# Kernel tuning notes

Hardware: AMD Instinct MI355X
Metric: run time of the kernel (lower is better)

Reference implementation:

```python
import jax, jax.numpy as jnp
import numpy as np

N_NODES = 50000


def gcn_conv_max(x, edge_index, edge_weight, W, b):
    """PyG GCNConv with aggr='max': gcn_norm (add self-loops, symmetric
    degree normalization), linear transform, gather-scale-scatter_max, bias."""
    n = x.shape[0]
    row, col = edge_index[0], edge_index[1]
    loop = jnp.arange(n)
    row = jnp.concatenate([row, loop])  # sources (incl. self-loops)
    col = jnp.concatenate([col, loop])  # targets
    ew = jnp.concatenate([edge_weight, jnp.ones((n,), x.dtype)])
    deg = jax.ops.segment_sum(ew, col, num_segments=n)
    dis = jnp.where(deg > 0, jax.lax.rsqrt(deg), jnp.zeros_like(deg))
    norm = dis[row] * ew * dis[col]  # [E+N]
    h = x @ W                         # [N, out]
    msg = norm[:, None] * h[row]      # gather + scale, [E+N, out]
    agg = jax.ops.segment_max(msg, col, num_segments=n)  # scatter-max
    return agg + b


def setup_inputs() -> dict:
    key = jax.random.key(0)
    ks = jax.random.split(key, 9)
    N, E = N_NODES, 1_600_000
    x = jax.random.normal(ks[0], (N, 5), dtype=jnp.float32)
    edge_index = jax.random.randint(ks[1], (2, E), 0, N, dtype=jnp.int64)
    edge_weight = jax.random.uniform(ks[2], (E,), dtype=jnp.float32)
    s1 = 1.0 / np.sqrt(5.0)
    s2 = 1.0 / np.sqrt(240.0)
    W1 = jax.random.uniform(ks[3], (5, 240), jnp.float32, -s1, s1)
    b1 = jnp.zeros((240,), jnp.float32)
    W2 = jax.random.uniform(ks[4], (240, 240), jnp.float32, -s2, s2)
    b2 = jnp.zeros((240,), jnp.float32)
    We = jax.random.uniform(ks[5], (240, 80), jnp.float32, -s2, s2)
    be = jnp.zeros((80,), jnp.float32)
    return {"x": x, "edge_index": edge_index, "edge_weight": edge_weight,
            "W1": W1, "b1": b1, "W2": W2, "b2": b2, "We": We, "be": be}


def reference(x, edge_index, edge_weight, W1, b1, W2, b2, We, be):
    h = gcn_conv_max(x, edge_index, edge_weight, W1, b1)
    h = jax.nn.relu(h)
    h = gcn_conv_max(h, edge_index, edge_weight, W2, b2)
    h = jax.nn.relu(h)
    return h @ We + be  # [N, 80]
```

## Files before the change

### kernel.cpp

```cpp
#include <hip/hip_runtime.h>
#include <cfloat>

#define HID 240

static inline size_t alignUp(size_t x, size_t a){ return (x + a - 1) / a * a; }

typedef __bf16 bf16x8 __attribute__((ext_vector_type(8)));
typedef unsigned short u16x8 __attribute__((ext_vector_type(8)));
typedef float  f32x16 __attribute__((ext_vector_type(16)));
typedef float  f32x4  __attribute__((ext_vector_type(4)));

__device__ __forceinline__ float b2f(unsigned short u){
    return __uint_as_float(((unsigned)u) << 16);
}
__device__ __forceinline__ unsigned short f2b_rne(float f){
    unsigned r = __float_as_uint(f);
    r += 0x7FFFu + ((r >> 16) & 1u);
    return (unsigned short)(r >> 16);
}
__device__ __forceinline__ float max3f(float a, float b, float c){
    return fmaxf(fmaxf(a, b), c);
}

__device__ __forceinline__ float vmax16(f32x16 a){
    float x0 = fmaxf(fmaxf(a[0],  a[1]),  a[2]);
    float x1 = fmaxf(fmaxf(a[3],  a[4]),  a[5]);
    float x2 = fmaxf(fmaxf(a[6],  a[7]),  a[8]);
    float x3 = fmaxf(fmaxf(a[9],  a[10]), a[11]);
    float x4 = fmaxf(fmaxf(a[12], a[13]), a[14]);
    float y0 = fmaxf(fmaxf(x0, x1), x2);
    float y1 = fmaxf(fmaxf(x3, x4), a[15]);
    return fmaxf(y0, y1);
}

__global__ void k_deg_prep(const int* __restrict__ col, const float* __restrict__ ew,
                           unsigned long long* __restrict__ pk, unsigned* __restrict__ rank,
                           int E, int ne, int N, int nb,
                           const float* __restrict__ x, float* __restrict__ xp,
                           const float* __restrict__ W1, unsigned short* __restrict__ W1f,
                           const float* __restrict__ W2, unsigned short* __restrict__ Bt2h,
                           unsigned short* __restrict__ Bt2l,
                           const float* __restrict__ We, unsigned short* __restrict__ Bt3h,
                           unsigned short* __restrict__ Bt3l){
    int b = blockIdx.x;
    int t = threadIdx.x;
    if (b < ne){
        int e = b * 256 + t;
        if (e < E){
            int c = col[e];
            unsigned q = __float2uint_rn(ew[e] * 1048576.0f);
            unsigned long long old = atomicAdd(&pk[c], (1ull << 40) | (unsigned long long)q);
            rank[e] = (unsigned)(old >> 40);
        }
        return;
    }
    int bb = b - ne;
    if (bb < nb){
        __shared__ float s[1280];
        int rbase = bb * 256;
        #pragma unroll
        for (int c = 0; c < 5; c++){
            int idx = rbase * 5 + t + 256 * c;
            s[t + 256 * c] = (idx < N * 5) ? x[idx] : 0.0f;
        }
        __syncthreads();
        #pragma unroll
        for (int c = 0; c < 8; c++){
            int pos = t + 256 * c;
            int r = pos >> 3, j = pos & 7;
            int grow = rbase + r;
            if (grow < N)
                xp[(size_t)grow * 8 + j] = (j < 5) ? s[r * 5 + j] : 0.0f;
        }
        return;
    }
    bb -= nb;
    if (bb < 32){
        int i = bb * 256 + t;
        if (i < 2 * 8 * 64 * 8){
            int k    = i & 7;
            int lane = (i >> 3) & 63;
            int j    = (i >> 9) & 7;
            int s2   = i >> 12;
            int lm = lane & 31, quad = lane >> 5;
            int kg = quad * 8 + k;
            int colm = 32 * j + lm;
            float v = (kg < 5 && colm < HID) ? W1[kg * HID + colm] : 0.0f;
            unsigned short hi = f2b_rne(v);
            W1f[i] = (s2 == 0) ? hi : f2b_rne(v - b2f(hi));
        }
        return;
    }
    bb -= 32;
    if (bb < 240){
        int i = bb * 256 + t;
        int n = i / HID, k = i - n * HID;
        float v = (n < HID) ? W2[(size_t)k * HID + n] : 0.0f;
        unsigned short hi = f2b_rne(v);
        Bt2h[i] = hi;
        Bt2l[i] = f2b_rne(v - b2f(hi));
        return;
    }
    bb -= 240;
    {
        int i = bb * 256 + t;
        if (i < 128 * HID){
            int n = i / HID, k = i - n * HID;
            float v = (n < 80) ? We[(size_t)k * 80 + n] : 0.0f;
            unsigned short hi = f2b_rne(v);
            Bt3h[i] = hi;
            Bt3l[i] = f2b_rne(v - b2f(hi));
        }
    }
}

__global__ void k_dis_bsum(const unsigned long long* __restrict__ pk,
                           float* __restrict__ dis, unsigned* __restrict__ cnt,
                           unsigned* __restrict__ bsum, int N){
    int b = blockIdx.x;
    int i = b * 256 + threadIdx.x;
    unsigned v = 0u;
    if (i < N){
        unsigned long long p = pk[i];
        unsigned c = (unsigned)(p >> 40);
        cnt[i] = c;
        float deg = 1.0f + (float)(p & 0xFFFFFFFFFFull) * (1.0f / 1048576.0f);
        dis[i] = rsqrtf(deg);
        v = (c + 32u) >> 5;
    }
    #pragma unroll
    for (int o = 32; o > 0; o >>= 1) v += __shfl_down(v, (unsigned)o, 64);
    __shared__ unsigned ws[4];
    int lane = threadIdx.x & 63, w = threadIdx.x >> 6;
    if (lane == 0) ws[w] = v;
    __syncthreads();
    if (threadIdx.x == 0) bsum[b] = ws[0] + ws[1] + ws[2] + ws[3];
}

__global__ void k_bscan(const unsigned* __restrict__ bsum, unsigned* __restrict__ boff,
                        unsigned* __restrict__ poff, int nb, int N){
    __shared__ unsigned s[256];
    int t = threadIdx.x;
    unsigned v = (t < nb) ? bsum[t] : 0u;
    s[t] = v;
    __syncthreads();
    for (int o = 1; o < 256; o <<= 1){
        unsigned u = (t >= o) ? s[t - o] : 0u;
        __syncthreads();
        s[t] += u;
        __syncthreads();
    }
    if (t < nb) boff[t] = s[t] - v;
    if (t == 0) poff[N] = 32u * s[nb - 1];
}

__global__ void k_offs_fill(const unsigned* __restrict__ cnt, const unsigned* __restrict__ boff,
                            const float* __restrict__ dis,
                            unsigned* __restrict__ poff, int2* __restrict__ sedge, int N){
    int b = blockIdx.x, t = threadIdx.x;
    int i = b * 256 + t;
    unsigned c = (i < N) ? cnt[i] : 0u;
    unsigned v = (i < N) ? ((c + 32u) >> 5) : 0u;
    int lane = t & 63, w = t >> 6;
    unsigned x = v;
    #pragma unroll
    for (int o = 1; o < 64; o <<= 1){
        unsigned u = __shfl_up(x, (unsigned)o, 64);
        if (lane >= o) x += u;
    }
    __shared__ unsigned ws[4];
    if (lane == 63) ws[w] = x;
    __syncthreads();
    unsigned wb = 0;
    if (w > 0) wb += ws[0];
    if (w > 1) wb += ws[1];
    if (w > 2) wb += ws[2];
    if (i < N){
        unsigned p = 32u * (boff[b] + wb + x - v);
        poff[i] = p;
        float dd = dis[i];
        int2 sv = make_int2(i, __float_as_int(dd * dd));
        sedge[p] = sv;
        unsigned s1 = p + 32u * v;
        for (unsigned s = p + 1u + c; s < s1; s++) sedge[s] = sv;
    }
}

__global__ void k_scatter(const int* __restrict__ row, const int* __restrict__ col,
                          const float* __restrict__ ew, const float* __restrict__ dis,
                          const unsigned* __restrict__ poff, const unsigned* __restrict__ rank,
                          int2* __restrict__ sedge, int E){
    int e = blockIdx.x * blockDim.x + threadIdx.x;
    if (e < E){
        int r = row[e], c = col[e];
        float nw = dis[r] * ew[e] * dis[c];
        unsigned p = poff[c] + 1u + rank[e];
        sedge[p] = make_int2(r, __float_as_int(nw));
    }
}

__global__ __launch_bounds__(256) void k_agg1m(const float* __restrict__ xp,
                                               const unsigned short* __restrict__ W1f,
                                               const unsigned* __restrict__ cnt,
                                               const unsigned* __restrict__ poff,
                                               const int2* __restrict__ sedge,
                                               const float* __restrict__ bias,
                                               float* __restrict__ out, int N, int nwaves){
    int wid  = blockIdx.x * 4 + (threadIdx.x >> 6);
    int lane = threadIdx.x & 63;
    int lm   = lane & 31;

    bf16x8 bh[8], bl[8];
    #pragma unroll
    for (int j = 0; j < 8; j++){
        bh[j] = *(const bf16x8*)(W1f + ((size_t)(0 * 8 + j) * 64 + lane) * 8);
        bl[j] = *(const bf16x8*)(W1f + ((size_t)(1 * 8 + j) * 64 + lane) * 8);
    }
    float bv[8];
    #pragma unroll
    for (int j = 0; j < 8; j++){
        int c = 32 * j + lm;
        bv[j] = (c < HID) ? bias[c] : 0.0f;
    }
    const f32x16 zv = {};

    for (int d = wid; d < N; d += nwaves){
        unsigned base = poff[d];
        unsigned nch  = (cnt[d] + 32u) >> 5;
        float m[8];
        #pragma unroll
        for (int j = 0; j < 8; j++) m[j] = -FLT_MAX;

        for (unsigned c = 0; c < nch; c++){
            u16x8 ahu = (u16x8)0, alu = (u16x8)0;
            if (lane < 32){
                int2 e = sedge[base + 32u * c + (unsigned)lm];
                float w = __int_as_float(e.y);
                const float4* xr = (const float4*)(xp + (size_t)e.x * 8);
                float4 x0 = xr[0], x1 = xr[1];
                float p[5] = {w * x0.x, w * x0.y, w * x0.z, w * x0.w, w * x1.x};
                #pragma unroll
                for (int k = 0; k < 5; k++){
                    unsigned short h = f2b_rne(p[k]);
                    ahu[k] = h;
                    alu[k] = f2b_rne(p[k] - b2f(h));
                }
            }
            bf16x8 ah = __builtin_bit_cast(bf16x8, ahu);
            bf16x8 al = __builtin_bit_cast(bf16x8, alu);
            #pragma unroll
            for (int j = 0; j < 8; j += 2){
                f32x16 a0 = __builtin_amdgcn_mfma_f32_32x32x16_bf16(ah, bh[j],     zv, 0, 0, 0);
                f32x16 a1 = __builtin_amdgcn_mfma_f32_32x32x16_bf16(ah, bh[j + 1], zv, 0, 0, 0);
                a0 = __builtin_amdgcn_mfma_f32_32x32x16_bf16(ah, bl[j],     a0, 0, 0, 0);
                a1 = __builtin_amdgcn_mfma_f32_32x32x16_bf16(ah, bl[j + 1], a1, 0, 0, 0);
                a0 = __builtin_amdgcn_mfma_f32_32x32x16_bf16(al, bh[j],     a0, 0, 0, 0);
                a1 = __builtin_amdgcn_mfma_f32_32x32x16_bf16(al, bh[j + 1], a1, 0, 0, 0);
                m[j]     = fmaxf(m[j],     vmax16(a0));
                m[j + 1] = fmaxf(m[j + 1], vmax16(a1));
            }
        }
        float o[8];
        #pragma unroll
        for (int j = 0; j < 8; j++){
            float other = __shfl_xor(m[j], 32, 64);
            o[j] = fmaxf(fmaxf(m[j], other) + bv[j], 0.0f);
        }
        if (lane < 32){
            float* orow = out + (size_t)d * HID;
            #pragma unroll
            for (int j = 0; j < 8; j++){
                int c = 32 * j + lm;
                if (c < HID) orow[c] = o[j];
            }
        }
    }
}

template <bool OB16>
__global__ __launch_bounds__(256) void k_gemm_mfma(const float* __restrict__ A,
                                                   const unsigned short* __restrict__ Bth,
                                                   const unsigned short* __restrict__ Btl,
                                                   const float* __restrict__ bias,
                                                   void* __restrict__ Cv,
                                                   int M, int Ncol, int Npad, int Cld){
    __shared__ unsigned short As_hi[64][24];
    __shared__ unsigned short As_lo[64][24];
    const int K = 240;
    int t = threadIdx.x;
    int wave = t >> 6, lane = t & 63;
    int m0 = blockIdx.x * 64;
    int n0 = wave * 64;
    bool wact = n0 < Npad;

    int lm   = lane & 31;
    int quad = lane >> 5;

    f32x16 acc[2][2] = {};

    for (int k0 = 0; k0 < K; k0 += 16){
        {
            int m = t >> 2, kq = (t & 3) * 4;
            float4 av = make_float4(0.f, 0.f, 0.f, 0.f);
            if (m0 + m < M) av = *(const float4*)(A + (size_t)(m0 + m) * K + k0 + kq);
            ushort4 hi, lo;
            hi.x = f2b_rne(av.x); lo.x = f2b_rne(av.x - b2f(hi.x));
            hi.y = f2b_rne(av.y); lo.y = f2b_rne(av.y - b2f(hi.y));
            hi.z = f2b_rne(av.z); lo.z = f2b_rne(av.z - b2f(hi.z));
            hi.w = f2b_rne(av.w); lo.w = f2b_rne(av.w - b2f(hi.w));
            *(ushort4*)&As_hi[m][kq] = hi;
            *(ushort4*)&As_lo[m][kq] = lo;
        }
        __syncthreads();
        if (wact){
            size_t bo0 = (size_t)(n0 + lm) * K + k0 + quad * 8;
            size_t bo1 = (size_t)(n0 + 32 + lm) * K + k0 + quad * 8;
            bf16x8 bh0 = *(const bf16x8*)(Bth + bo0);
            bf16x8 bl0 = *(const bf16x8*)(Btl + bo0);
            bf16x8 bh1 = *(const bf16x8*)(Bth + bo1);
            bf16x8 bl1 = *(const bf16x8*)(Btl + bo1);
            #pragma unroll
            for (int mh = 0; mh < 2; mh++){
                bf16x8 ah = *(const bf16x8*)&As_hi[32 * mh + lm][quad * 8];
                bf16x8 al = *(const bf16x8*)&As_lo[32 * mh + lm][quad * 8];
                acc[mh][0] = __builtin_amdgcn_mfma_f32_32x32x16_bf16(ah, bh0, acc[mh][0], 0, 0, 0);
                acc[mh][0] = __builtin_amdgcn_mfma_f32_32x32x16_bf16(ah, bl0, acc[mh][0], 0, 0, 0);
                acc[mh][0] = __builtin_amdgcn_mfma_f32_32x32x16_bf16(al, bh0, acc[mh][0], 0, 0, 0);
                acc[mh][1] = __builtin_amdgcn_mfma_f32_32x32x16_bf16(ah, bh1, acc[mh][1], 0, 0, 0);
                acc[mh][1] = __builtin_amdgcn_mfma_f32_32x32x16_bf16(ah, bl1, acc[mh][1], 0, 0, 0);
                acc[mh][1] = __builtin_amdgcn_mfma_f32_32x32x16_bf16(al, bh1, acc[mh][1], 0, 0, 0);
            }
        }
        __syncthreads();
    }

    if (!wact) return;
    #pragma unroll
    for (int mh = 0; mh < 2; mh++){
        #pragma unroll
        for (int h = 0; h < 2; h++){
            int n = n0 + 32 * h + lm;
            if (n >= Ncol) continue;
            float bvv = (!OB16 && bias) ? bias[n] : 0.0f;
            #pragma unroll
            for (int r = 0; r < 16; r++){
                int m = m0 + 32 * mh + (r & 3) + 8 * (r >> 2) + 4 * quad;
                if (m >= M) continue;
                float v = acc[mh][h][r];
                if (OB16){
                    ((unsigned short*)Cv)[(size_t)m * Cld + n] = f2b_rne(v);
                } else {
                    ((float*)Cv)[(size_t)m * Cld + n] = v + bvv;
                }
            }
        }
    }
}

__global__ __launch_bounds__(256) void k_aggb(const unsigned short* __restrict__ H2,
                                              const unsigned* __restrict__ cnt,
                                              const unsigned* __restrict__ poff,
                                              const int2* __restrict__ sedge,
                                              const float* __restrict__ bias,
                                              float* __restrict__ out, int N){
    int d    = blockIdx.x * 4 + (threadIdx.x >> 6);
    int lane = threadIdx.x & 63;
    if (d >= N) return;
    bool act = lane < 60;

    unsigned p0  = poff[d];
    unsigned ng8 = (cnt[d] + 8u) >> 3;
    const int2* se = sedge + p0;

    float4 m = make_float4(-FLT_MAX, -FLT_MAX, -FLT_MAX, -FLT_MAX);
    for (unsigned it = 0; it < ng8; it++){
        int2 e0 = se[0], e1 = se[1], e2 = se[2], e3 = se[3];
        int2 e4 = se[4], e5 = se[5], e6 = se[6], e7 = se[7];
        se += 8;
        if (act){
            ushort4 g0 = ((const ushort4*)(H2 + ((size_t)(unsigned)e0.x << 8)))[lane];
            ushort4 g1 = ((const ushort4*)(H2 + ((size_t)(unsigned)e1.x << 8)))[lane];
            ushort4 g2 = ((const ushort4*)(H2 + ((size_t)(unsigned)e2.x << 8)))[lane];
            ushort4 g3 = ((const ushort4*)(H2 + ((size_t)(unsigned)e3.x << 8)))[lane];
            ushort4 g4 = ((const ushort4*)(H2 + ((size_t)(unsigned)e4.x << 8)))[lane];
            ushort4 g5 = ((const ushort4*)(H2 + ((size_t)(unsigned)e5.x << 8)))[lane];
            ushort4 g6 = ((const ushort4*)(H2 + ((size_t)(unsigned)e6.x << 8)))[lane];
            ushort4 g7 = ((const ushort4*)(H2 + ((size_t)(unsigned)e7.x << 8)))[lane];
            float w0 = __int_as_float(e0.y), w1 = __int_as_float(e1.y);
            float w2 = __int_as_float(e2.y), w3 = __int_as_float(e3.y);
            float w4 = __int_as_float(e4.y), w5 = __int_as_float(e5.y);
            float w6 = __int_as_float(e6.y), w7 = __int_as_float(e7.y);
            m.x = max3f(max3f(w0*b2f(g0.x), w1*b2f(g1.x), w2*b2f(g2.x)),
                        max3f(w3*b2f(g3.x), w4*b2f(g4.x), w5*b2f(g5.x)),
                        max3f(w6*b2f(g6.x), w7*b2f(g7.x), m.x));
            m.y = max3f(max3f(w0*b2f(g0.y), w1*b2f(g1.y), w2*b2f(g2.y)),
                        max3f(w3*b2f(g3.y), w4*b2f(g4.y), w5*b2f(g5.y)),
                        max3f(w6*b2f(g6.y), w7*b2f(g7.y), m.y));
            m.z = max3f(max3f(w0*b2f(g0.z), w1*b2f(g1.z), w2*b2f(g2.z)),
                        max3f(w3*b2f(g3.z), w4*b2f(g4.z), w5*b2f(g5.z)),
                        max3f(w6*b2f(g6.z), w7*b2f(g7.z), m.z));
            m.w = max3f(max3f(w0*b2f(g0.w), w1*b2f(g1.w), w2*b2f(g2.w)),
                        max3f(w3*b2f(g3.w), w4*b2f(g4.w), w5*b2f(g5.w)),
                        max3f(w6*b2f(g6.w), w7*b2f(g7.w), m.w));
        }
    }
    if (act){
        float4 b = ((const float4*)bias)[lane];
        float4 o;
        o.x = fmaxf(m.x + b.x, 0.0f);
        o.y = fmaxf(m.y + b.y, 0.0f);
        o.z = fmaxf(m.z + b.z, 0.0f);
        o.w = fmaxf(m.w + b.w, 0.0f);
        ((float4*)(out + (size_t)d * HID))[lane] = o;
    }
}

extern "C" void kernel_launch(void* const* d_in, const int* in_sizes, int n_in,
                              void* d_out, int out_size, void* d_ws, size_t ws_size,
                              hipStream_t stream){
    const float* x  = (const float*)d_in[0];
    const int*   ei = (const int*)  d_in[1];
    const float* ew = (const float*)d_in[2];
    const float* W1 = (const float*)d_in[3];
    const float* b1 = (const float*)d_in[4];
    const float* W2 = (const float*)d_in[5];
    const float* b2 = (const float*)d_in[6];
    const float* We = (const float*)d_in[7];
    const float* be = (const float*)d_in[8];
    float* out = (float*)d_out;

    const int N = in_sizes[0] / 5;
    const int E = in_sizes[2];
    const int* row = ei;
    const int* col = ei + E;
    const int nb = (N + 255) / 256;

    char* w = (char*)d_ws;
    size_t o = 0;
    auto alloc = [&](size_t bytes) -> void* {
        void* p = w + o;
        o = alignUp(o + bytes, 256);
        return p;
    };
    unsigned long long* pk = (unsigned long long*) alloc((size_t)N * 8);
    float*          dis   = (float*)          alloc((size_t)N * 4);
    unsigned*       cnt   = (unsigned*)       alloc((size_t)N * 4);
    unsigned*       poff  = (unsigned*)       alloc((size_t)(N + 1) * 4);
    unsigned*       bsum  = (unsigned*)       alloc((size_t)nb * 4);
    unsigned*       boff  = (unsigned*)       alloc((size_t)nb * 4);
    unsigned*       rank  = (unsigned*)       alloc((size_t)E * 4);
    int2*           sedge = (int2*)           alloc(((size_t)E + 32u * N + 64u) * 8);
    float*          xp    = (float*)          alloc((size_t)N * 8 * 4);
    unsigned short* W1f   = (unsigned short*) alloc((size_t)2 * 8 * 64 * 8 * 2);
    unsigned short* Bt2h  = (unsigned short*) alloc((size_t)256 * HID * 2);
    unsigned short* Bt2l  = (unsigned short*) alloc((size_t)256 * HID * 2);
    unsigned short* Bt3h  = (unsigned short*) alloc((size_t)128 * HID * 2);
    unsigned short* Bt3l  = (unsigned short*) alloc((size_t)128 * HID * 2);
    unsigned short* bufH2 = (unsigned short*) alloc((size_t)N * 256 * 2);
    float*          bufB  = (float*)          alloc((size_t)N * HID * 4);
    (void)ws_size; (void)n_in; (void)out_size;

    int ne = (E + 255) / 256;

    hipMemsetAsync(pk, 0, (size_t)N * 8, stream);
    k_deg_prep <<<ne + nb + 32 + 240 + 120, 256, 0, stream>>>(col, ew, pk, rank, E, ne, N, nb,
                                                              x, xp, W1, W1f,
                                                              W2, Bt2h, Bt2l,
                                                              We, Bt3h, Bt3l);
    k_dis_bsum <<<nb, 256, 0, stream>>>(pk, dis, cnt, bsum, N);
    k_bscan    <<<1, 256, 0, stream>>>(bsum, boff, poff, nb, N);
    k_offs_fill<<<nb, 256, 0, stream>>>(cnt, boff, dis, poff, sedge, N);
    k_scatter  <<<ne, 256, 0, stream>>>(row, col, ew, dis, poff, rank, sedge, E);

    const int a1blocks = 1536;
    k_agg1m<<<a1blocks, 256, 0, stream>>>(xp, W1f, cnt, poff, sedge, b1, bufB, N, a1blocks * 4);

    int gm = (N + 63) / 64;
    k_gemm_mfma<true><<<gm, 256, 0, stream>>>(bufB, Bt2h, Bt2l, nullptr, bufH2, N, HID, 256, 256);
    k_aggb<<<(N + 3) / 4, 256, 0, stream>>>(bufH2, cnt, poff, sedge, b2, bufB, N);

    k_gemm_mfma<false><<<gm, 256, 0, stream>>>(bufB, Bt3h, Bt3l, be, out, N, 80, 128, 80);
}
```

Baseline: 485.3 us.

## Fuse second max-aggregation with final linear layer via in-block MFMA

The second-layer gather/scatter-max now writes each node's ReLU'd row into shared memory as split bf16 hi/lo values rather than fp32 to global memory. The same block then runs the 240→80 output projection with 16x16x32 bf16 MFMAs on its 16 rows and writes the result directly. This removes the fp32 intermediate round trip through global memory and one kernel launch. In exchange each wave handles four destination nodes in sequence, there are fewer blocks, and the B-fragment loads read slightly past column 240, relying on the zero-padded A columns to cancel them.

```diff
diff --git a/kernel.cpp b/kernel.cpp
--- a/kernel.cpp
+++ b/kernel.cpp
@@ -357,61 +357,115 @@
     }
 }
 
-__global__ __launch_bounds__(256) void k_aggb(const unsigned short* __restrict__ H2,
-                                              const unsigned* __restrict__ cnt,
-                                              const unsigned* __restrict__ poff,
-                                              const int2* __restrict__ sedge,
-                                              const float* __restrict__ bias,
-                                              float* __restrict__ out, int N){
-    int d    = blockIdx.x * 4 + (threadIdx.x >> 6);
-    int lane = threadIdx.x & 63;
-    if (d >= N) return;
+__global__ __launch_bounds__(256) void k_aggb_f(const unsigned short* __restrict__ H2,
+                                                const unsigned* __restrict__ cnt,
+                                                const unsigned* __restrict__ poff,
+                                                const int2* __restrict__ sedge,
+                                                const float* __restrict__ bias,
+                                                const unsigned short* __restrict__ Bt3h,
+                                                const unsigned short* __restrict__ Bt3l,
+                                                const float* __restrict__ be,
+                                                float* __restrict__ out, int N){
+    __shared__ unsigned short Ah[16][264];
+    __shared__ unsigned short Al[16][264];
+
+    int t    = threadIdx.x;
+    int wid  = t >> 6;
+    int lane = t & 63;
+    int tbase = blockIdx.x * 16;
+
+    for (int i = t; i < 16 * 24; i += 256){
+        int r = i / 24, c = 240 + (i % 24);
+        Ah[r][c] = 0;
+        Al[r][c] = 0;
+    }
+
     bool act = lane < 60;
-
-    unsigned p0  = poff[d];
-    unsigned ng8 = (cnt[d] + 8u) >> 3;
-    const int2* se = sedge + p0;
-
-    float4 m = make_float4(-FLT_MAX, -FLT_MAX, -FLT_MAX, -FLT_MAX);
-    for (unsigned it = 0; it < ng8; it++){
-        int2 e0 = se[0], e1 = se[1], e2 = se[2], e3 = se[3];
-        int2 e4 = se[4], e5 = se[5], e6 = se[6], e7 = se[7];
-        se += 8;
-        if (act){
-            ushort4 g0 = ((const ushort4*)(H2 + ((size_t)(unsigned)e0.x << 8)))[lane];
-            ushort4 g1 = ((const ushort4*)(H2 + ((size_t)(unsigned)e1.x << 8)))[lane];
-            ushort4 g2 = ((const ushort4*)(H2 + ((size_t)(unsigned)e2.x << 8)))[lane];
-            ushort4 g3 = ((const ushort4*)(H2 + ((size_t)(unsigned)e3.x << 8)))[lane];
-            ushort4 g4 = ((const ushort4*)(H2 + ((size_t)(unsigned)e4.x << 8)))[lane];
-            ushort4 g5 = ((const ushort4*)(H2 + ((size_t)(unsigned)e5.x << 8)))[lane];
-            ushort4 g6 = ((const ushort4*)(H2 + ((size_t)(unsigned)e6.x << 8)))[lane];
-            ushort4 g7 = ((const ushort4*)(H2 + ((size_t)(unsigned)e7.x << 8)))[lane];
-            float w0 = __int_as_float(e0.y), w1 = __int_as_float(e1.y);
-            float w2 = __int_as_float(e2.y), w3 = __int_as_float(e3.y);
-            float w4 = __int_as_float(e4.y), w5 = __int_as_float(e5.y);
-            float w6 = __int_as_float(e6.y), w7 = __int_as_float(e7.y);
-            m.x = max3f(max3f(w0*b2f(g0.x), w1*b2f(g1.x), w2*b2f(g2.x)),
-                        max3f(w3*b2f(g3.x), w4*b2f(g4.x), w5*b2f(g5.x)),
-                        max3f(w6*b2f(g6.x), w7*b2f(g7.x), m.x));
-            m.y = max3f(max3f(w0*b2f(g0.y), w1*b2f(g1.y), w2*b2f(g2.y)),
-                        max3f(w3*b2f(g3.y), w4*b2f(g4.y), w5*b2f(g5.y)),
-                        max3f(w6*b2f(g6.y), w7*b2f(g7.y), m.y));
-            m.z = max3f(max3f(w0*b2f(g0.z), w1*b2f(g1.z), w2*b2f(g2.z)),
-                        max3f(w3*b2f(g3.z), w4*b2f(g4.z), w5*b2f(g5.z)),
-                        max3f(w6*b2f(g6.z), w7*b2f(g7.z), m.z));
-            m.w = max3f(max3f(w0*b2f(g0.w), w1*b2f(g1.w), w2*b2f(g2.w)),
-                        max3f(w3*b2f(g3.w), w4*b2f(g4.w), w5*b2f(g5.w)),
-                        max3f(w6*b2f(g6.w), w7*b2f(g7.w), m.w));
-        }
-    }
-    if (act){
-        float4 b = ((const float4*)bias)[lane];
-        float4 o;
-        o.x = fmaxf(m.x + b.x, 0.0f);
-        o.y = fmaxf(m.y + b.y, 0.0f);
-        o.z = fmaxf(m.z + b.z, 0.0f);
-        o.w = fmaxf(m.w + b.w, 0.0f);
-        ((float4*)(out + (size_t)d * HID))[lane] = o;
+    float4 bv = act ? ((const float4*)bias)[lane] : make_float4(0.f, 0.f, 0.f, 0.f);
+    #pragma unroll
+    for (int i = 0; i < 4; i++){
+        int rowi = wid * 4 + i;
+        int d = tbase + rowi;
+        unsigned p0  = (d < N) ? poff[d] : 0u;
+        unsigned ng8 = (d < N) ? ((cnt[d] + 8u) >> 3) : 0u;
+        const int2* se = sedge + p0;
+
+        float4 m = make_float4(-FLT_MAX, -FLT_MAX, -FLT_MAX, -FLT_MAX);
+        for (unsigned it = 0; it < ng8; it++){
+            int2 e0 = se[0], e1 = se[1], e2 = se[2], e3 = se[3];
+            int2 e4 = se[4], e5 = se[5], e6 = se[6], e7 = se[7];
+            se += 8;
+            if (act){
+                ushort4 g0 = ((const ushort4*)(H2 + ((size_t)(unsigned)e0.x << 8)))[lane];
+                ushort4 g1 = ((const ushort4*)(H2 + ((size_t)(unsigned)e1.x << 8)))[lane];
+                ushort4 g2 = ((const ushort4*)(H2 + ((size_t)(unsigned)e2.x << 8)))[lane];
+                ushort4 g3 = ((const ushort4*)(H2 + ((size_t)(unsigned)e3.x << 8)))[lane];
+                ushort4 g4 = ((const ushort4*)(H2 + ((size_t)(unsigned)e4.x << 8)))[lane];
+                ushort4 g5 = ((const ushort4*)(H2 + ((size_t)(unsigned)e5.x << 8)))[lane];
+                ushort4 g6 = ((const ushort4*)(H2 + ((size_t)(unsigned)e6.x << 8)))[lane];
+                ushort4 g7 = ((const ushort4*)(H2 + ((size_t)(unsigned)e7.x << 8)))[lane];
+                float w0 = __int_as_float(e0.y), w1 = __int_as_float(e1.y);
+                float w2 = __int_as_float(e2.y), w3 = __int_as_float(e3.y);
+                float w4 = __int_as_float(e4.y), w5 = __int_as_float(e5.y);
+                float w6 = __int_as_float(e6.y), w7 = __int_as_float(e7.y);
+                m.x = max3f(max3f(w0*b2f(g0.x), w1*b2f(g1.x), w2*b2f(g2.x)),
+                            max3f(w3*b2f(g3.x), w4*b2f(g4.x), w5*b2f(g5.x)),
+                            max3f(w6*b2f(g6.x), w7*b2f(g7.x), m.x));
+                m.y = max3f(max3f(w0*b2f(g0.y), w1*b2f(g1.y), w2*b2f(g2.y)),
+                            max3f(w3*b2f(g3.y), w4*b2f(g4.y), w5*b2f(g5.y)),
+                            max3f(w6*b2f(g6.y), w7*b2f(g7.y), m.y));
+                m.z = max3f(max3f(w0*b2f(g0.z), w1*b2f(g1.z), w2*b2f(g2.z)),
+                            max3f(w3*b2f(g3.z), w4*b2f(g4.z), w5*b2f(g5.z)),
+                            max3f(w6*b2f(g6.z), w7*b2f(g7.z), m.z));
+                m.w = max3f(max3f(w0*b2f(g0.w), w1*b2f(g1.w), w2*b2f(g2.w)),
+                            max3f(w3*b2f(g3.w), w4*b2f(g4.w), w5*b2f(g5.w)),
+                            max3f(w6*b2f(g6.w), w7*b2f(g7.w), m.w));
+            }
+        }
+        if (act && (d < N)){
+            float o0 = fmaxf(m.x + bv.x, 0.0f);
+            float o1 = fmaxf(m.y + bv.y, 0.0f);
+            float o2 = fmaxf(m.z + bv.z, 0.0f);
+            float o3 = fmaxf(m.w + bv.w, 0.0f);
+            ushort4 hi, lo;
+            hi.x = f2b_rne(o0); lo.x = f2b_rne(o0 - b2f(hi.x));
+            hi.y = f2b_rne(o1); lo.y = f2b_rne(o1 - b2f(hi.y));
+            hi.z = f2b_rne(o2); lo.z = f2b_rne(o2 - b2f(hi.z));
+            hi.w = f2b_rne(o3); lo.w = f2b_rne(o3 - b2f(hi.w));
+            *(ushort4*)&Ah[rowi][lane * 4] = hi;
+            *(ushort4*)&Al[rowi][lane * 4] = lo;
+        } else if (act){
+            ushort4 z = make_ushort4(0, 0, 0, 0);
+            *(ushort4*)&Ah[rowi][lane * 4] = z;
+            *(ushort4*)&Al[rowi][lane * 4] = z;
+        }
+    }
+    __syncthreads();
+
+    int arow = lane & 15;
+    int kgrp = (lane >> 4) * 8;
+    for (int tile = wid; tile < 5; tile += 4){
+        int n0 = tile * 16;
+        int coln = n0 + (lane & 15);
+        f32x4 acc = {};
+        #pragma unroll
+        for (int kk = 0; kk < 256; kk += 32){
+            bf16x8 ah = *(const bf16x8*)&Ah[arow][kk + kgrp];
+            bf16x8 al = *(const bf16x8*)&Al[arow][kk + kgrp];
+            bf16x8 bh = *(const bf16x8*)(Bt3h + (size_t)coln * 240 + kk + kgrp);
+            bf16x8 bl = *(const bf16x8*)(Bt3l + (size_t)coln * 240 + kk + kgrp);
+            acc = __builtin_amdgcn_mfma_f32_16x16x32_bf16(ah, bh, acc, 0, 0, 0);
+            acc = __builtin_amdgcn_mfma_f32_16x16x32_bf16(ah, bl, acc, 0, 0, 0);
+            acc = __builtin_amdgcn_mfma_f32_16x16x32_bf16(al, bh, acc, 0, 0, 0);
+        }
+        float bev = be[coln];
+        #pragma unroll
+        for (int r = 0; r < 4; r++){
+            int mrow = (lane >> 4) * 4 + r;
+            int d2 = tbase + mrow;
+            if (d2 < N)
+                out[(size_t)d2 * 80 + coln] = acc[r] + bev;
+        }
     }
 }
 
@@ -477,7 +531,7 @@
 
     int gm = (N + 63) / 64;
     k_gemm_mfma<true><<<gm, 256, 0, stream>>>(bufB, Bt2h, Bt2l, nullptr, bufH2, N, HID, 256, 256);
-    k_aggb<<<(N + 3) / 4, 256, 0, stream>>>(bufH2, cnt, poff, sedge, b2, bufB, N);
-
-    k_gemm_mfma<false><<<gm, 256, 0, stream>>>(bufB, Bt3h, Bt3l, be, out, N, 80, 128, 80);
-}
+
+    k_aggb_f<<<(N + 15) / 16, 256, 0, stream>>>(bufH2, cnt, poff, sedge, b2,
+                                                Bt3h, Bt3l, be, out, N);
+}
```

Result: faster. 452.0 us (-6.8%).
